# Kernel optimization log

Hardware: AMD Instinct MI355X
Metric: run time of the kernel (lower is better)

Reference implementation:

```python
import jax, jax.numpy as jnp
import numpy as np
from jax import lax

B, T_SRC, C_IN = 32, 1024, 512
CH, T_DE = 256, 4096
K, K_EMB = 5, 3
LEAKY = 0.3
EPS = 1e-5


def setup_inputs() -> dict:
    key = jax.random.key(0)
    ks = jax.random.split(key, 8)
    s = 0.02
    return {
        "x": jax.random.normal(ks[0], (B, T_SRC, C_IN), jnp.float32),
        "target": jax.random.normal(ks[1], (B, 1, T_DE), jnp.float32),
        "dr": jax.random.randint(ks[2], (B, T_SRC), 0, 4),
        "mask": jnp.zeros((B, T_SRC), bool),
        "w_conv1": jax.random.normal(ks[3], (CH, C_IN, K), jnp.float32) * s,
        "b_conv1": jnp.zeros((CH,), jnp.float32),
        "ln1_g": jnp.ones((CH,), jnp.float32),
        "ln1_b": jnp.zeros((CH,), jnp.float32),
        "w_conv2": jax.random.normal(ks[4], (CH, CH, K), jnp.float32) * s,
        "b_conv2": jnp.zeros((CH,), jnp.float32),
        "ln2_g": jnp.ones((CH,), jnp.float32),
        "ln2_b": jnp.zeros((CH,), jnp.float32),
        "w_lin": jax.random.normal(ks[5], (CH, 1), jnp.float32) * s,
        "b_lin": jnp.zeros((1,), jnp.float32),
        "w_emb": jax.random.normal(ks[6], (CH, 1, K_EMB), jnp.float32) * s,
        "b_emb": jnp.zeros((CH,), jnp.float32),
    }


def _conv1d(x, w, b, pad):
    # x: [B, C_in, T], w: [C_out, C_in, K]
    y = lax.conv_general_dilated(x, w, (1,), [(pad, pad)], dimension_numbers=("NCH", "OIH", "NCH"))
    return y + b[None, :, None]


def _layernorm(x, g, b):
    m = jnp.mean(x, -1, keepdims=True)
    v = jnp.var(x, -1, keepdims=True)
    return (x - m) * lax.rsqrt(v + EPS) * g + b


def _average_over_durations(values, durs):
    # values: [B, 1, T_de], durs: [B, T_en] -> [B, 1, T_en]
    ends = jnp.cumsum(durs, 1)                                   # [B, T_en]
    starts = jnp.pad(ends[:, :-1], ((0, 0), (1, 0)))
    nz_cum = jnp.pad(jnp.cumsum((values != 0.0).astype(jnp.float32), 2), ((0, 0), (0, 0), (1, 0)))
    v_cum = jnp.pad(jnp.cumsum(values, 2), ((0, 0), (0, 0), (1, 0)))
    dce = ends[:, None, :]
    dcs = starts[:, None, :]
    sums = jnp.take_along_axis(v_cum, dce, 2) - jnp.take_along_axis(v_cum, dcs, 2)
    nel = jnp.take_along_axis(nz_cum, dce, 2) - jnp.take_along_axis(nz_cum, dcs, 2)
    return jnp.where(nel == 0.0, 0.0, sums / nel)


def reference(x, target, dr, mask, w_conv1, b_conv1, ln1_g, ln1_b, w_conv2, b_conv2, ln2_g, ln2_b, w_lin, b_lin, w_emb, b_emb):
    # VariancePredictor: [conv -> leaky_relu -> layernorm] x2 -> linear -> mask (eval mode, dropout off)
    h = _conv1d(x.transpose(0, 2, 1), w_conv1, b_conv1, (K - 1) // 2).transpose(0, 2, 1)
    h = _layernorm(jax.nn.leaky_relu(h, LEAKY), ln1_g, ln1_b)
    h = _conv1d(h.transpose(0, 2, 1), w_conv2, b_conv2, (K - 1) // 2).transpose(0, 2, 1)
    h = _layernorm(jax.nn.leaky_relu(h, LEAKY), ln2_g, ln2_b)
    energy_pred = (h @ w_lin + b_lin)[..., 0]                     # [B, T_src]
    energy_pred = jnp.where(mask, 0.0, energy_pred)
    avg_energy_target = _average_over_durations(target, dr)       # [B, 1, T_src]
    energy_emb = _conv1d(avg_energy_target, w_emb, b_emb, (K_EMB - 1) // 2)  # [B, CH, T_src]
    return energy_pred, avg_energy_target, energy_emb
```

## Files before the change

### kernel.cpp

```cpp
#include <hip/hip_runtime.h>

typedef __attribute__((ext_vector_type(8))) short short8;
typedef __attribute__((ext_vector_type(4))) float f32x4;

#define LEAKY_F 0.3f

typedef __attribute__((address_space(3))) void lds_t;
typedef __attribute__((address_space(1))) void gmem_t;
#define G2L(g, l) __builtin_amdgcn_global_load_lds((const gmem_t*)(g), (lds_t*)(l), 16, 0, 0)

__device__ __forceinline__ unsigned short f2bf(float f) {
    union { float f; unsigned u; } v; v.f = f;
    unsigned u = v.u;
    return (unsigned short)((u + 0x7fffu + ((u >> 16) & 1u)) >> 16);
}
__device__ __forceinline__ float bf2f(unsigned short u) {
    union { unsigned u; float f; } v; v.u = ((unsigned)u) << 16; return v.f;
}

__global__ void cast_pad_x(const float* __restrict__ in, unsigned short* __restrict__ out) {
    int i = blockIdx.x * 256 + threadIdx.x;
    long g = (long)i * 8;
    int row = (int)(g >> 9);
    int b = row >> 10;
    long o = ((long)(row + (b << 2) + 2) << 9) + (g & 511);
    const float4* p = (const float4*)(in + g);
    float4 a = p[0], c = p[1];
    union { unsigned short s[8]; uint4 v; } u;
    u.s[0] = f2bf(a.x); u.s[1] = f2bf(a.y); u.s[2] = f2bf(a.z); u.s[3] = f2bf(a.w);
    u.s[4] = f2bf(c.x); u.s[5] = f2bf(c.y); u.s[6] = f2bf(c.z); u.s[7] = f2bf(c.w);
    *(uint4*)(out + o) = u.v;
}

__global__ void zero_pads(unsigned short* __restrict__ p, int cin) {
    int j = blockIdx.x * 256 + threadIdx.x;
    int upb = cin >> 1;
    int b = j / upb, rem = j % upb;
    int upr = cin >> 3;
    int r4 = rem / upr;
    int col = (rem % upr) * 8;
    int rowp = (r4 < 2) ? r4 : (r4 + 1024);
    *(uint4*)(p + ((long)b * 1028 + rowp) * cin + col) = make_uint4(0u, 0u, 0u, 0u);
}

__global__ void prep_w(const float* __restrict__ w, unsigned short* __restrict__ out, int CIN, int n) {
    int i = blockIdx.x * 256 + threadIdx.x;
    if (i >= n) return;
    int ch = i / (CIN * 5);
    int rem = i % (CIN * 5);
    int tap = rem / CIN;
    int cin = rem % CIN;
    out[ch * (5 * CIN) + tap * CIN + cin] = f2bf(w[(ch * CIN + cin) * 5 + tap]);
}

template<int CIN, bool PRED>
__global__ __launch_bounds__(512, 2) void gemm_conv_fused(
    const unsigned short* __restrict__ A,
    const unsigned short* __restrict__ W,
    const float* __restrict__ bias,
    const float* __restrict__ gam,
    const float* __restrict__ bet,
    const float* __restrict__ wlin,
    const float* __restrict__ blin,
    const unsigned char* __restrict__ mask,
    unsigned short* __restrict__ Yln,
    float* __restrict__ Ypred)
{
    constexpr int KW = 5 * CIN;
    constexpr int S  = KW / 64;
    constexpr int ASLOT = 128 * 64;
    constexpr int BSLOT = 256 * 64;
    __shared__ __align__(16) unsigned short smem[3 * (ASLOT + BSLOT)];
    __shared__ float pb[1024];

    const int tid = threadIdx.x, lane = tid & 63, wid = tid >> 6;
    const int wm = wid >> 2, wn = wid & 3;
    const int blk = blockIdx.x;
    const int bb = blk >> 3, tl0 = (blk & 7) << 7;
    const long rowbase = (long)bb * 1028 + tl0;

    long asrc[2]; int adst[2];
    #pragma unroll
    for (int c = 0; c < 2; c++) {
        int u = ((c * 8 + wid) << 6) + lane;
        int r = u >> 3, sg = (u & 7) ^ (r & 7);
        asrc[c] = (rowbase + r) * (long)CIN + sg * 8;
        adst[c] = (c * 8 + wid) << 9;
    }
    long bsrc[4]; int bdst[4];
    #pragma unroll
    for (int c = 0; c < 4; c++) {
        int u = ((c * 8 + wid) << 6) + lane;
        int r = u >> 3, sg = (u & 7) ^ (r & 7);
        bsrc[c] = (long)r * KW + sg * 8;
        bdst[c] = (c * 8 + wid) << 9;
    }

    auto stage = [&](int t, int slot) {
        const int k0 = t * 64;
        unsigned short* a = smem + slot * ASLOT;
        unsigned short* b = smem + 3 * ASLOT + slot * BSLOT;
        #pragma unroll
        for (int c = 0; c < 2; c++) G2L(A + asrc[c] + k0, a + adst[c]);
        #pragma unroll
        for (int c = 0; c < 4; c++) G2L(W + bsrc[c] + k0, b + bdst[c]);
    };

    const int l15 = lane & 15, lhi = (lane >> 4) & 3, sw = l15 & 7;
    const int arow = (wm * 64 + l15) * 64;
    const int brow = (wn * 64 + l15) * 64;
    const int sg0 = ((lhi ^ sw) & 7) << 3;
    const int sg1 = (((4 | lhi) ^ sw) & 7) << 3;

    f32x4 acc[4][4] = {};

    stage(0, 0);
    stage(1, 1);

    int rb = 0;
    #pragma unroll 1
    for (int t = 0; t < S; ++t) {
        if (t < S - 1) { asm volatile("s_waitcnt vmcnt(6)" ::: "memory"); }
        else           { asm volatile("s_waitcnt vmcnt(0)" ::: "memory"); }
        __builtin_amdgcn_sched_barrier(0);
        __builtin_amdgcn_s_barrier();
        __builtin_amdgcn_sched_barrier(0);

        const unsigned short* ab = smem + rb * ASLOT;
        const unsigned short* bp = smem + 3 * ASLOT + rb * BSLOT;

        short8 af0[4], bg0[4], af1[4], bg1[4];
        #pragma unroll
        for (int m = 0; m < 4; m++)
            af0[m] = *(const short8*)&ab[arow + m * 1024 + sg0];
        #pragma unroll
        for (int n = 0; n < 4; n++)
            bg0[n] = *(const short8*)&bp[brow + n * 1024 + sg0];

        if (t + 2 < S) stage(t + 2, (rb == 0) ? 2 : (rb - 1));

        #pragma unroll
        for (int m = 0; m < 4; m++)
            af1[m] = *(const short8*)&ab[arow + m * 1024 + sg1];
        #pragma unroll
        for (int n = 0; n < 4; n++)
            bg1[n] = *(const short8*)&bp[brow + n * 1024 + sg1];

        asm volatile("s_waitcnt lgkmcnt(8)" ::: "memory");
        __builtin_amdgcn_sched_barrier(0);
        __builtin_amdgcn_s_setprio(1);
        #pragma unroll
        for (int m = 0; m < 4; m++)
            #pragma unroll
            for (int n = 0; n < 4; n++)
                acc[m][n] = __builtin_amdgcn_mfma_f32_16x16x32_bf16(af0[m], bg0[n], acc[m][n], 0, 0, 0);
        __builtin_amdgcn_s_setprio(0);
        __builtin_amdgcn_sched_barrier(0);

        asm volatile("s_waitcnt lgkmcnt(0)" ::: "memory");
        __builtin_amdgcn_sched_barrier(0);
        __builtin_amdgcn_s_setprio(1);
        #pragma unroll
        for (int m = 0; m < 4; m++)
            #pragma unroll
            for (int n = 0; n < 4; n++)
                acc[m][n] = __builtin_amdgcn_mfma_f32_16x16x32_bf16(af1[m], bg1[n], acc[m][n], 0, 0, 0);
        __builtin_amdgcn_s_setprio(0);
        __builtin_amdgcn_sched_barrier(0);

        rb = (rb == 2) ? 0 : (rb + 1);
    }

    __syncthreads();

    if (tid < 256) {
        pb[tid]       = bias[tid];
        pb[256 + tid] = gam[tid];
        pb[512 + tid] = bet[tid];
        pb[768 + tid] = PRED ? wlin[tid] : 0.f;
    }
    __syncthreads();

    unsigned short* tile = smem;
    #pragma unroll
    for (int n = 0; n < 4; n++) {
        const int col = wn * 64 + n * 16 + l15;
        const float bv = pb[col];
        const int u0 = col >> 3, ce = col & 7;
        #pragma unroll
        for (int m = 0; m < 4; m++) {
            const int rA = wm * 64 + m * 16 + lhi * 4;
            #pragma unroll
            for (int q = 0; q < 4; q++) {
                const int row = rA + q;
                float v = acc[m][n][q] + bv;
                v = v > 0.f ? v : LEAKY_F * v;
                tile[row * 256 + ((u0 ^ (row & 7)) << 3) + ce] = f2bf(v);
            }
        }
    }
    __syncthreads();

    const int rid = tid >> 2, jq = tid & 3;
    const int r7 = rid & 7;
    float vals[8][8];
    float s1 = 0.f, s2 = 0.f, sgw = 0.f, sgc = 0.f, sbw = 0.f;
    #pragma unroll
    for (int u4 = 0; u4 < 8; u4++) {
        const int u = u4 * 4 + jq;
        short8 pk = *(const short8*)&tile[rid * 256 + ((u ^ r7) << 3)];
        #pragma unroll
        for (int e = 0; e < 8; e++) {
            float v = bf2f((unsigned short)pk[e]);
            vals[u4][e] = v;
            s1 += v; s2 += v * v;
        }
        if (PRED) {
            const int c0 = u * 8;
            f32x4 ga = *(const f32x4*)&pb[256 + c0], gb = *(const f32x4*)&pb[260 + c0];
            f32x4 wa = *(const f32x4*)&pb[768 + c0], wb = *(const f32x4*)&pb[772 + c0];
            f32x4 ba = *(const f32x4*)&pb[512 + c0], bb2 = *(const f32x4*)&pb[516 + c0];
            #pragma unroll
            for (int e = 0; e < 4; e++) {
                sgw += vals[u4][e] * ga[e] * wa[e] + vals[u4][e + 4] * gb[e] * wb[e];
                sgc += ga[e] * wa[e] + gb[e] * wb[e];
                sbw += ba[e] * wa[e] + bb2[e] * wb[e];
            }
        }
    }
    s1 += __shfl_xor(s1, 1); s1 += __shfl_xor(s1, 2);
    s2 += __shfl_xor(s2, 1); s2 += __shfl_xor(s2, 2);
    const float mean = s1 * (1.f / 256.f);
    const float var  = s2 * (1.f / 256.f) - mean * mean;
    const float rs   = rsqrtf(var + 1e-5f);
    const long grow  = (long)blk * 128 + rid;

    if (PRED) {
        sgw += __shfl_xor(sgw, 1); sgw += __shfl_xor(sgw, 2);
        sgc += __shfl_xor(sgc, 1); sgc += __shfl_xor(sgc, 2);
        sbw += __shfl_xor(sbw, 1); sbw += __shfl_xor(sbw, 2);
        if (jq == 0) {
            float p = rs * (sgw - mean * sgc) + sbw + blin[0];
            if (mask[grow]) p = 0.f;
            Ypred[grow] = p;
        }
    } else {
        const int bnum = (int)(grow >> 10);
        const long prow = grow + (bnum << 2) + 2;
        #pragma unroll
        for (int u4 = 0; u4 < 8; u4++) {
            const int u = u4 * 4 + jq;
            const int c0 = u * 8;
            f32x4 ga = *(const f32x4*)&pb[256 + c0], gb = *(const f32x4*)&pb[260 + c0];
            f32x4 ba = *(const f32x4*)&pb[512 + c0], bb2 = *(const f32x4*)&pb[516 + c0];
            union { unsigned short s[8]; uint4 v; } o;
            #pragma unroll
            for (int e = 0; e < 4; e++) {
                o.s[e]     = f2bf((vals[u4][e]     - mean) * rs * ga[e] + ba[e]);
                o.s[e + 4] = f2bf((vals[u4][e + 4] - mean) * rs * gb[e] + bb2[e]);
            }
            *(uint4*)(Yln + prow * 256 + c0) = o.v;
        }
    }
}

__global__ void avg_kernel(const float* __restrict__ target, const int* __restrict__ dr,
                           float* __restrict__ outAvg) {
    __shared__ float vcum[4097];
    __shared__ float ncum[4097];
    __shared__ float sS[256];
    __shared__ float sC[256];
    __shared__ int   sI[256];
    int b = blockIdx.x, tid = threadIdx.x;
    const float* tb = target + b * 4096;
    float lv[16]; float ls = 0.f, lc = 0.f;
    #pragma unroll
    for (int j = 0; j < 16; j++) {
        float v = tb[tid * 16 + j]; lv[j] = v; ls += v; lc += (v != 0.f) ? 1.f : 0.f;
    }
    sS[tid] = ls; sC[tid] = lc;
    __syncthreads();
    for (int off = 1; off < 256; off <<= 1) {
        float a = 0.f, c2 = 0.f;
        if (tid >= off) { a = sS[tid - off]; c2 = sC[tid - off]; }
        __syncthreads();
        sS[tid] += a; sC[tid] += c2;
        __syncthreads();
    }
    float pS = tid ? sS[tid - 1] : 0.f, pC = tid ? sC[tid - 1] : 0.f;
    if (tid == 0) { vcum[0] = 0.f; ncum[0] = 0.f; }
    float run = pS, runc = pC;
    #pragma unroll
    for (int j = 0; j < 16; j++) {
        run += lv[j]; runc += (lv[j] != 0.f) ? 1.f : 0.f;
        vcum[tid * 16 + j + 1] = run; ncum[tid * 16 + j + 1] = runc;
    }
    const int* db = dr + b * 1024;
    int ld[4]; int lsum = 0;
    #pragma unroll
    for (int j = 0; j < 4; j++) { ld[j] = db[tid * 4 + j]; lsum += ld[j]; }
    sI[tid] = lsum;
    __syncthreads();
    for (int off = 1; off < 256; off <<= 1) {
        int a = 0; if (tid >= off) a = sI[tid - off];
        __syncthreads();
        sI[tid] += a;
        __syncthreads();
    }
    int run2 = tid ? sI[tid - 1] : 0;
    #pragma unroll
    for (int j = 0; j < 4; j++) {
        run2 += ld[j];
        int e = run2, s0 = e - ld[j];
        float sums = vcum[e] - vcum[s0];
        float cnt  = ncum[e] - ncum[s0];
        outAvg[b * 1024 + tid * 4 + j] = (cnt == 0.f) ? 0.f : sums / cnt;
    }
}

__global__ void emb_kernel(const float* __restrict__ avg, const float* __restrict__ wemb,
                           const float* __restrict__ bemb, float* __restrict__ out) {
    int id = blockIdx.x * 256 + threadIdx.x;
    int t4 = id & 255;
    int ch = (id >> 8) & 255;
    int b  = id >> 16;
    int t0 = t4 * 4;
    const float* a = avg + b * 1024;
    float am1 = (t0 - 1 >= 0) ? a[t0 - 1] : 0.f;
    float a0 = a[t0], a1 = a[t0 + 1], a2 = a[t0 + 2], a3 = a[t0 + 3];
    float a4 = (t0 + 4 < 1024) ? a[t0 + 4] : 0.f;
    float w0 = wemb[ch * 3], w1 = wemb[ch * 3 + 1], w2 = wemb[ch * 3 + 2], bb = bemb[ch];
    float4 o;
    o.x = bb + am1 * w0 + a0 * w1 + a1 * w2;
    o.y = bb + a0 * w0 + a1 * w1 + a2 * w2;
    o.z = bb + a1 * w0 + a2 * w1 + a3 * w2;
    o.w = bb + a2 * w0 + a3 * w1 + a4 * w2;
    *(float4*)(out + (((b << 8) | ch) << 10) + t0) = o;
}

extern "C" void kernel_launch(void* const* d_in, const int* in_sizes, int n_in,
                              void* d_out, int out_size, void* d_ws, size_t ws_size,
                              hipStream_t stream) {
    const float* x      = (const float*)d_in[0];
    const float* target = (const float*)d_in[1];
    const int*   dr     = (const int*)d_in[2];
    const unsigned char* mask = (const unsigned char*)d_in[3];
    const float* w1   = (const float*)d_in[4];
    const float* b1   = (const float*)d_in[5];
    const float* g1   = (const float*)d_in[6];
    const float* be1  = (const float*)d_in[7];
    const float* w2   = (const float*)d_in[8];
    const float* b2   = (const float*)d_in[9];
    const float* g2   = (const float*)d_in[10];
    const float* be2  = (const float*)d_in[11];
    const float* wlin = (const float*)d_in[12];
    const float* blin = (const float*)d_in[13];
    const float* wemb = (const float*)d_in[14];
    const float* bemb = (const float*)d_in[15];

    char* ws = (char*)d_ws;
    unsigned short* xbp  = (unsigned short*)ws;
    unsigned short* h1bp = (unsigned short*)(ws + 33685504);
    unsigned short* wr1  = (unsigned short*)(ws + 50528256);
    unsigned short* wr2  = (unsigned short*)(ws + 51838976);

    float* outPred = (float*)d_out;
    float* outAvg  = outPred + 32768;
    float* outEmb  = outPred + 65536;

    cast_pad_x<<<8192, 256, 0, stream>>>(x, xbp);
    zero_pads<<<32, 256, 0, stream>>>(xbp, 512);
    zero_pads<<<16, 256, 0, stream>>>(h1bp, 256);
    prep_w<<<2560, 256, 0, stream>>>(w1, wr1, 512, 256 * 512 * 5);
    prep_w<<<1280, 256, 0, stream>>>(w2, wr2, 256, 256 * 256 * 5);
    gemm_conv_fused<512, false><<<256, 512, 0, stream>>>(
        xbp, wr1, b1, g1, be1, wlin, blin, mask, h1bp, outPred);
    gemm_conv_fused<256, true><<<256, 512, 0, stream>>>(
        h1bp, wr2, b2, g2, be2, wlin, blin, mask, h1bp, outPred);
    avg_kernel<<<32, 256, 0, stream>>>(target, dr, outAvg);
    emb_kernel<<<8192, 256, 0, stream>>>(outAvg, wemb, bemb, outEmb);
}
```

Measured before the change: 135.7 us.

## Retile fused conv GEMM to 64-row blocks of 256 threads with K-step 32

Shrinks the fused conv-GEMM block tile from 128x256 with 512 threads and a 64-wide K step to 64x256 with 256 threads and a 32-wide K step. The grid doubles to 512 blocks, and the LDS swizzle, staging addresses and wait counts are rewritten for the narrower slices. The aim is finer-grained scheduling, with smaller blocks and less LDS per block that can be placed more flexibly across CUs. In exchange, weight tiles are reloaded twice as often from global memory, and there are twice as many barrier-separated K iterations, each with less MFMA work to hide latency.

```diff
diff --git a/kernel.cpp b/kernel.cpp
--- a/kernel.cpp
+++ b/kernel.cpp
@@ -54,7 +54,7 @@
 }
 
 template<int CIN, bool PRED>
-__global__ __launch_bounds__(512, 2) void gemm_conv_fused(
+__global__ __launch_bounds__(256, 2) void gemm_conv_fused(
     const unsigned short* __restrict__ A,
     const unsigned short* __restrict__ W,
     const float* __restrict__ bias,
@@ -67,50 +67,43 @@
     float* __restrict__ Ypred)
 {
     constexpr int KW = 5 * CIN;
-    constexpr int S  = KW / 64;
-    constexpr int ASLOT = 128 * 64;
-    constexpr int BSLOT = 256 * 64;
+    constexpr int S  = KW / 32;
+    constexpr int ASLOT = 64 * 32;
+    constexpr int BSLOT = 256 * 32;
     __shared__ __align__(16) unsigned short smem[3 * (ASLOT + BSLOT)];
     __shared__ float pb[1024];
 
-    const int tid = threadIdx.x, lane = tid & 63, wid = tid >> 6;
-    const int wm = wid >> 2, wn = wid & 3;
+    const int tid = threadIdx.x, lane = tid & 63, wn = tid >> 6;
     const int blk = blockIdx.x;
-    const int bb = blk >> 3, tl0 = (blk & 7) << 7;
+    const int bb = blk >> 4, tl0 = (blk & 15) << 6;
     const long rowbase = (long)bb * 1028 + tl0;
 
-    long asrc[2]; int adst[2];
-    #pragma unroll
-    for (int c = 0; c < 2; c++) {
-        int u = ((c * 8 + wid) << 6) + lane;
-        int r = u >> 3, sg = (u & 7) ^ (r & 7);
-        asrc[c] = (rowbase + r) * (long)CIN + sg * 8;
-        adst[c] = (c * 8 + wid) << 9;
+    long asrc; int adst;
+    {
+        int r = tid >> 2, q = tid & 3, sg = q ^ (r & 3);
+        asrc = (rowbase + r) * (long)CIN + sg * 8;
+        adst = tid * 8;
     }
     long bsrc[4]; int bdst[4];
     #pragma unroll
     for (int c = 0; c < 4; c++) {
-        int u = ((c * 8 + wid) << 6) + lane;
-        int r = u >> 3, sg = (u & 7) ^ (r & 7);
+        int u = c * 256 + tid;
+        int r = u >> 2, q = u & 3, sg = q ^ (r & 3);
         bsrc[c] = (long)r * KW + sg * 8;
-        bdst[c] = (c * 8 + wid) << 9;
+        bdst[c] = u * 8;
     }
 
     auto stage = [&](int t, int slot) {
-        const int k0 = t * 64;
-        unsigned short* a = smem + slot * ASLOT;
+        const int k0 = t * 32;
+        G2L(A + asrc + k0, &smem[slot * ASLOT + adst]);
         unsigned short* b = smem + 3 * ASLOT + slot * BSLOT;
-        #pragma unroll
-        for (int c = 0; c < 2; c++) G2L(A + asrc[c] + k0, a + adst[c]);
         #pragma unroll
         for (int c = 0; c < 4; c++) G2L(W + bsrc[c] + k0, b + bdst[c]);
     };
 
-    const int l15 = lane & 15, lhi = (lane >> 4) & 3, sw = l15 & 7;
-    const int arow = (wm * 64 + l15) * 64;
-    const int brow = (wn * 64 + l15) * 64;
-    const int sg0 = ((lhi ^ sw) & 7) << 3;
-    const int sg1 = (((4 | lhi) ^ sw) & 7) << 3;
+    const int l15 = lane & 15, lhi = (lane >> 4) & 3;
+    const int sgoff = ((lhi ^ (l15 & 3)) & 3) << 3;
+    const int brow0 = wn * 64;
 
     f32x4 acc[4][4] = {};
 
@@ -120,7 +113,7 @@
     int rb = 0;
     #pragma unroll 1
     for (int t = 0; t < S; ++t) {
-        if (t < S - 1) { asm volatile("s_waitcnt vmcnt(6)" ::: "memory"); }
+        if (t < S - 1) { asm volatile("s_waitcnt vmcnt(5)" ::: "memory"); }
         else           { asm volatile("s_waitcnt vmcnt(0)" ::: "memory"); }
         __builtin_amdgcn_sched_barrier(0);
         __builtin_amdgcn_s_barrier();
@@ -128,57 +121,36 @@
 
         const unsigned short* ab = smem + rb * ASLOT;
         const unsigned short* bp = smem + 3 * ASLOT + rb * BSLOT;
-
-        short8 af0[4], bg0[4], af1[4], bg1[4];
+        short8 af[4], bg[4];
         #pragma unroll
         for (int m = 0; m < 4; m++)
-            af0[m] = *(const short8*)&ab[arow + m * 1024 + sg0];
+            af[m] = *(const short8*)&ab[(m * 16 + l15) * 32 + sgoff];
         #pragma unroll
         for (int n = 0; n < 4; n++)
-            bg0[n] = *(const short8*)&bp[brow + n * 1024 + sg0];
+            bg[n] = *(const short8*)&bp[(brow0 + n * 16 + l15) * 32 + sgoff];
 
         if (t + 2 < S) stage(t + 2, (rb == 0) ? 2 : (rb - 1));
 
-        #pragma unroll
-        for (int m = 0; m < 4; m++)
-            af1[m] = *(const short8*)&ab[arow + m * 1024 + sg1];
-        #pragma unroll
-        for (int n = 0; n < 4; n++)
-            bg1[n] = *(const short8*)&bp[brow + n * 1024 + sg1];
-
-        asm volatile("s_waitcnt lgkmcnt(8)" ::: "memory");
+        asm volatile("s_waitcnt lgkmcnt(0)" ::: "memory");
         __builtin_amdgcn_sched_barrier(0);
         __builtin_amdgcn_s_setprio(1);
         #pragma unroll
         for (int m = 0; m < 4; m++)
             #pragma unroll
             for (int n = 0; n < 4; n++)
-                acc[m][n] = __builtin_amdgcn_mfma_f32_16x16x32_bf16(af0[m], bg0[n], acc[m][n], 0, 0, 0);
+                acc[m][n] = __builtin_amdgcn_mfma_f32_16x16x32_bf16(af[m], bg[n], acc[m][n], 0, 0, 0);
         __builtin_amdgcn_s_setprio(0);
         __builtin_amdgcn_sched_barrier(0);
 
-        asm volatile("s_waitcnt lgkmcnt(0)" ::: "memory");
-        __builtin_amdgcn_sched_barrier(0);
-        __builtin_amdgcn_s_setprio(1);
-        #pragma unroll
-        for (int m = 0; m < 4; m++)
-            #pragma unroll
-            for (int n = 0; n < 4; n++)
-                acc[m][n] = __builtin_amdgcn_mfma_f32_16x16x32_bf16(af1[m], bg1[n], acc[m][n], 0, 0, 0);
-        __builtin_amdgcn_s_setprio(0);
-        __builtin_amdgcn_sched_barrier(0);
-
         rb = (rb == 2) ? 0 : (rb + 1);
     }
 
     __syncthreads();
 
-    if (tid < 256) {
-        pb[tid]       = bias[tid];
-        pb[256 + tid] = gam[tid];
-        pb[512 + tid] = bet[tid];
-        pb[768 + tid] = PRED ? wlin[tid] : 0.f;
-    }
+    pb[tid]       = bias[tid];
+    pb[256 + tid] = gam[tid];
+    pb[512 + tid] = bet[tid];
+    pb[768 + tid] = PRED ? wlin[tid] : 0.f;
     __syncthreads();
 
     unsigned short* tile = smem;
@@ -189,7 +161,7 @@
         const int u0 = col >> 3, ce = col & 7;
         #pragma unroll
         for (int m = 0; m < 4; m++) {
-            const int rA = wm * 64 + m * 16 + lhi * 4;
+            const int rA = m * 16 + lhi * 4;
             #pragma unroll
             for (int q = 0; q < 4; q++) {
                 const int row = rA + q;
@@ -233,7 +205,7 @@
     const float mean = s1 * (1.f / 256.f);
     const float var  = s2 * (1.f / 256.f) - mean * mean;
     const float rs   = rsqrtf(var + 1e-5f);
-    const long grow  = (long)blk * 128 + rid;
+    const long grow  = (long)blk * 64 + rid;
 
     if (PRED) {
         sgw += __shfl_xor(sgw, 1); sgw += __shfl_xor(sgw, 2);
@@ -373,9 +345,9 @@
     zero_pads<<<16, 256, 0, stream>>>(h1bp, 256);
     prep_w<<<2560, 256, 0, stream>>>(w1, wr1, 512, 256 * 512 * 5);
     prep_w<<<1280, 256, 0, stream>>>(w2, wr2, 256, 256 * 256 * 5);
-    gemm_conv_fused<512, false><<<256, 512, 0, stream>>>(
+    gemm_conv_fused<512, false><<<512, 256, 0, stream>>>(
         xbp, wr1, b1, g1, be1, wlin, blin, mask, h1bp, outPred);
-    gemm_conv_fused<256, true><<<256, 512, 0, stream>>>(
+    gemm_conv_fused<256, true><<<512, 256, 0, stream>>>(
         h1bp, wr2, b2, g2, be2, wlin, blin, mask, h1bp, outPred);
     avg_kernel<<<32, 256, 0, stream>>>(target, dr, outAvg);
     emb_kernel<<<8192, 256, 0, stream>>>(outAvg, wemb, bemb, outEmb);
```

Measured after the change: 142.4 us. 4.9% more time.
